# Performance work log

Hardware: AMD Instinct MI355X
Metric: run time of the kernel (lower is better)

Reference implementation:

```python
import jax, jax.numpy as jnp
import numpy as np

L, S, N, E, H = 1024, 1024, 4, 1024, 16


def setup_inputs() -> dict:
    key = jax.random.key(0)
    ks = jax.random.split(key, 7)
    return {
        "query": jax.random.normal(ks[0], (L, N, E), jnp.float32),
        "key": jax.random.normal(ks[1], (S, N, E), jnp.float32),
        "value": jax.random.normal(ks[2], (S, N, E), jnp.float32),
        "in_proj_weight": jax.random.normal(ks[3], (3 * E, E), jnp.float32) * (E ** -0.5),
        "in_proj_bias": jax.random.normal(ks[4], (3 * E,), jnp.float32) * 0.02,
        "out_proj_weight": jax.random.normal(ks[5], (E, E), jnp.float32) * (E ** -0.5),
        "out_proj_bias": jax.random.normal(ks[6], (E,), jnp.float32) * 0.02,
        "num_heads": H,
    }


def _split_heads(x, n, h, hd):
    # (T, N, E) -> (N*h, T, hd), matching torch view(T, N*h, hd).transpose(0, 1)
    t = x.shape[0]
    return jnp.transpose(x.reshape(t, n * h, hd), (1, 0, 2))


def reference(query, key, value, in_proj_weight, in_proj_bias,
              out_proj_weight, out_proj_bias, num_heads):
    tgt_len, bsz, embed_dim = query.shape
    src_len = key.shape[0]
    head_dim = embed_dim // num_heads
    scaling = float(head_dim) ** -0.5

    # packed QKV projection (torch F.linear: x @ W.T + b), sliced as in source
    q = query @ in_proj_weight[:embed_dim].T + in_proj_bias[:embed_dim]
    k = key @ in_proj_weight[embed_dim:2 * embed_dim].T + in_proj_bias[embed_dim:2 * embed_dim]
    v = value @ in_proj_weight[2 * embed_dim:].T + in_proj_bias[2 * embed_dim:]
    q = q * scaling

    q = _split_heads(q, bsz, num_heads, head_dim)  # (N*H, L, hd)
    k = _split_heads(k, bsz, num_heads, head_dim)  # (N*H, S, hd)
    v = _split_heads(v, bsz, num_heads, head_dim)  # (N*H, S, hd)

    scores = jnp.einsum('bld,bsd->bls', q, k)           # (N*H, L, S)
    attn = jax.nn.softmax(scores, axis=-1)
    ctx = jnp.einsum('bls,bsd->bld', attn, v)           # (N*H, L, hd)

    # (N*H, L, hd) -> (L, N, E)
    ctx = jnp.transpose(ctx, (1, 0, 2)).reshape(tgt_len, bsz, embed_dim)
    attn_output = ctx @ out_proj_weight.T + out_proj_bias

    # need_weights=True path: average over heads -> (N, L, S)
    attn_weights = attn.reshape(bsz, num_heads, tgt_len, src_len).sum(axis=1) / num_heads
    return attn_output, attn_weights
```

## Files before the change

kernel.cpp:

```cpp
#include <hip/hip_runtime.h>

typedef unsigned short u16;
typedef __attribute__((ext_vector_type(8))) short short8;
typedef __attribute__((ext_vector_type(4))) float f32x4;

__device__ __forceinline__ u16 f2bf(float f) {
  unsigned int i = __float_as_uint(f);
  i += 0x7fffu + ((i >> 16) & 1u);
  return (u16)(i >> 16);
}

__device__ __forceinline__ short8 cvt8(const float* p) {
  float4 a = ((const float4*)p)[0];
  float4 b = ((const float4*)p)[1];
  short8 r;
  r[0] = (short)f2bf(a.x); r[1] = (short)f2bf(a.y);
  r[2] = (short)f2bf(a.z); r[3] = (short)f2bf(a.w);
  r[4] = (short)f2bf(b.x); r[5] = (short)f2bf(b.y);
  r[6] = (short)f2bf(b.z); r[7] = (short)f2bf(b.w);
  return r;
}

__global__ __launch_bounds__(256) void convert_bf16(
    const float* __restrict__ q, const float* __restrict__ k,
    const float* __restrict__ v, const float* __restrict__ Wi,
    const float* __restrict__ Wo,
    u16* __restrict__ qb, u16* __restrict__ kb, u16* __restrict__ vb,
    u16* __restrict__ Wib, u16* __restrict__ Wob)
{
  const float* src; u16* dst; int len8;
  switch (blockIdx.y) {
    case 0:  src = q;  dst = qb;  len8 = 524288; break;
    case 1:  src = k;  dst = kb;  len8 = 524288; break;
    case 2:  src = v;  dst = vb;  len8 = 524288; break;
    case 3:  src = Wi; dst = Wib; len8 = 393216; break;
    default: src = Wo; dst = Wob; len8 = 131072; break;
  }
  int stride = gridDim.x * 256;
  for (int i = blockIdx.x * 256 + threadIdx.x; i < len8; i += stride)
    *(short8*)(dst + (size_t)i * 8) = cvt8(src + (size_t)i * 8);
}

__global__ __launch_bounds__(256) void qkv_gemm(
    const u16* __restrict__ qb, const u16* __restrict__ kb,
    const u16* __restrict__ vb, const u16* __restrict__ W,
    const float* __restrict__ bias,
    u16* __restrict__ qh, u16* __restrict__ kh, u16* __restrict__ vt)
{
  __shared__ __align__(16) u16 As[128 * 64];
  __shared__ __align__(16) u16 Bs[128 * 64];

  const int tid  = threadIdx.x;
  const int wave = tid >> 6;
  const int lane = tid & 63;
  const int r    = lane & 15;
  const int q4   = lane >> 4;
  const int wm   = wave >> 1;
  const int wn   = wave & 1;

  const int orig = blockIdx.y * 24 + blockIdx.x;
  const int nid  = (orig & 7) * 96 + (orig >> 3);
  const int mt   = nid / 24;
  const int jt   = nid - mt * 24;
  const int src  = jt >> 3;
  const u16* X = (src == 0) ? qb : (src == 1) ? kb : vb;
  const int m0 = mt * 128;
  const int j0 = jt * 128;

  const int ls   = lane >> 3;
  const int swzb = ((lane & 7) ^ ls) << 4;
  const char* Xc = (const char*)X;
  const char* Wc = (const char*)W;

  f32x4 acc[4][4];
  #pragma unroll
  for (int a = 0; a < 4; ++a)
    #pragma unroll
    for (int b = 0; b < 4; ++b)
      acc[a][b] = (f32x4){0.f, 0.f, 0.f, 0.f};

  for (int kt = 0; kt < 16; ++kt) {
    const int kb2 = kt * 128;
    __syncthreads();
    #pragma unroll
    for (int i = 0; i < 4; ++i) {
      const int row = wave * 32 + i * 8 + ls;
      __builtin_amdgcn_global_load_lds(
          (const u16*)(Xc + (size_t)(m0 + row) * 2048 + kb2 + swzb),
          As + (wave * 4 + i) * 512, 16, 0, 0);
      __builtin_amdgcn_global_load_lds(
          (const u16*)(Wc + (size_t)(j0 + row) * 2048 + kb2 + swzb),
          Bs + (wave * 4 + i) * 512, 16, 0, 0);
    }
    __syncthreads();

    #pragma unroll
    for (int ks = 0; ks < 2; ++ks) {
      short8 af[4], bf[4];
      #pragma unroll
      for (int mi = 0; mi < 4; ++mi) {
        const int row = wm * 64 + mi * 16 + r;
        af[mi] = *(const short8*)(As + row * 64 + ((((ks << 2) | q4) ^ (r & 7)) << 3));
      }
      #pragma unroll
      for (int ji = 0; ji < 4; ++ji) {
        const int row = wn * 64 + ji * 16 + r;
        bf[ji] = *(const short8*)(Bs + row * 64 + ((((ks << 2) | q4) ^ (r & 7)) << 3));
      }
      #pragma unroll
      for (int mi = 0; mi < 4; ++mi)
        #pragma unroll
        for (int ji = 0; ji < 4; ++ji)
          acc[mi][ji] = __builtin_amdgcn_mfma_f32_16x16x32_bf16(af[mi], bf[ji], acc[mi][ji], 0, 0, 0);
    }
  }

  #pragma unroll
  for (int mi = 0; mi < 4; ++mi) {
    #pragma unroll
    for (int ji = 0; ji < 4; ++ji) {
      #pragma unroll
      for (int rr = 0; rr < 4; ++rr) {
        int m = m0 + wm * 64 + mi * 16 + q4 * 4 + rr;
        int j = j0 + wn * 64 + ji * 16 + r;
        float v = acc[mi][ji][rr] + bias[j];
        int t = m >> 2, n = m & 3;
        int jj = j & 1023;
        int h = jj >> 6, d = jj & 63;
        int bb = n * 16 + h;
        if (src == 0)
          qh[(size_t)bb * 65536 + (size_t)t * 64 + d] = f2bf(v * 0.125f);
        else if (src == 1)
          kh[(size_t)bb * 65536 + (size_t)t * 64 + d] = f2bf(v);
        else
          vt[(size_t)bb * 65536 + (size_t)d * 1024 + t] = f2bf(v);
      }
    }
  }
}

__global__ __launch_bounds__(256) void attn_ctx_mfma(
    const u16* __restrict__ qh, const u16* __restrict__ kh,
    const u16* __restrict__ vt, u16* __restrict__ ctx,
    float* __restrict__ Zbuf)
{
  __shared__ __align__(16) u16 Ks[2][4096];
  __shared__ __align__(16) u16 Vs[2][4096];
  __shared__ __align__(16) u16 Pl[4][1024];

  const int tid = threadIdx.x;
  const int wv = tid >> 6, lane = tid & 63, r = lane & 15, q4 = lane >> 4;
  const int b  = blockIdx.y;
  const int lw = blockIdx.x * 64 + wv * 16;
  const int n = b >> 4, h = b & 15;

  const u16* qbase = qh + (size_t)b * 65536;
  const char* kc = (const char*)(kh + (size_t)b * 65536);
  const char* vc = (const char*)(vt + (size_t)b * 65536);
  u16* P = Pl[wv];

  const int ls  = lane >> 3;
  const int swzb = ((lane & 7) ^ ls) << 4;
  const int iw  = wv * 2;
  const size_t klo = (size_t)iw * 1024 + (size_t)ls * 128 + swzb;
  const size_t vlo = (size_t)iw * 16384 + (size_t)ls * 2048 + swzb;

  const int rsw = r & 7;
  const int c0 = (q4 ^ rsw) << 3;
  const int c1 = ((q4 ^ rsw) ^ 4) << 3;

  short8 aq0 = *(const short8*)(qbase + (size_t)(lw + r) * 64 + q4 * 8);
  short8 aq1 = *(const short8*)(qbase + (size_t)(lw + r) * 64 + 32 + q4 * 8);

  f32x4 oc[4];
  #pragma unroll
  for (int ji = 0; ji < 4; ++ji) oc[ji] = (f32x4){0.f, 0.f, 0.f, 0.f};
  float z[4] = {0.f, 0.f, 0.f, 0.f};

  {
    const char* kp = kc + klo;
    const char* vp = vc + vlo;
    u16* kd = &Ks[0][iw * 512];
    u16* vd = &Vs[0][iw * 512];
    __builtin_amdgcn_global_load_lds(kp,          kd,       16, 0, 0);
    __builtin_amdgcn_global_load_lds(kp + 1024,   kd + 512, 16, 0, 0);
    __builtin_amdgcn_global_load_lds(vp,          vd,       16, 0, 0);
    __builtin_amdgcn_global_load_lds(vp + 16384,  vd + 512, 16, 0, 0);
  }

  for (int it = 0; it < 16; ++it) {
    const int cur = it & 1;
    __syncthreads();
    const u16* Kb = Ks[cur];
    const u16* Vb = Vs[cur];

    f32x4 sc[4];
    #pragma unroll
    for (int ji = 0; ji < 4; ++ji) {
      const int row = (ji * 16 + r) * 64;
      short8 bk0 = *(const short8*)(Kb + row + c0);
      short8 bk1 = *(const short8*)(Kb + row + c1);
      f32x4 t = (f32x4){0.f, 0.f, 0.f, 0.f};
      t = __builtin_amdgcn_mfma_f32_16x16x32_bf16(aq0, bk0, t, 0, 0, 0);
      t = __builtin_amdgcn_mfma_f32_16x16x32_bf16(aq1, bk1, t, 0, 0, 0);
      sc[ji] = t;
    }

    if (it < 15) {
      const char* kp = kc + (size_t)(it + 1) * 8192 + klo;
      const char* vp = vc + (size_t)(it + 1) * 128  + vlo;
      u16* kd = &Ks[cur ^ 1][iw * 512];
      u16* vd = &Vs[cur ^ 1][iw * 512];
      __builtin_amdgcn_global_load_lds(kp,          kd,       16, 0, 0);
      __builtin_amdgcn_global_load_lds(kp + 1024,   kd + 512, 16, 0, 0);
      __builtin_amdgcn_global_load_lds(vp,          vd,       16, 0, 0);
      __builtin_amdgcn_global_load_lds(vp + 16384,  vd + 512, 16, 0, 0);
    }

    #pragma unroll
    for (int ji = 0; ji < 4; ++ji) {
      const int cw = ji * 2 + (r >> 3);
      #pragma unroll
      for (int rr = 0; rr < 4; ++rr) {
        float e = __expf(sc[ji][rr]);
        z[rr] += e;
        const int row = q4 * 4 + rr;
        P[row * 64 + ((cw ^ (row & 7)) << 3) + (r & 7)] = f2bf(e);
      }
    }
    asm volatile("s_waitcnt lgkmcnt(0)" ::: "memory");
    short8 ap0 = *(const short8*)(P + r * 64 + c0);
    short8 ap1 = *(const short8*)(P + r * 64 + c1);
    #pragma unroll
    for (int ji = 0; ji < 4; ++ji) {
      const int row = (ji * 16 + r) * 64;
      short8 bv0 = *(const short8*)(Vb + row + c0);
      short8 bv1 = *(const short8*)(Vb + row + c1);
      oc[ji] = __builtin_amdgcn_mfma_f32_16x16x32_bf16(ap0, bv0, oc[ji], 0, 0, 0);
      oc[ji] = __builtin_amdgcn_mfma_f32_16x16x32_bf16(ap1, bv1, oc[ji], 0, 0, 0);
    }
  }

  #pragma unroll
  for (int rr = 0; rr < 4; ++rr) {
    float zz = z[rr];
    zz += __shfl_xor(zz, 1);
    zz += __shfl_xor(zz, 2);
    zz += __shfl_xor(zz, 4);
    zz += __shfl_xor(zz, 8);
    z[rr] = zz;
  }

  #pragma unroll
  for (int rr = 0; rr < 4; ++rr) {
    float inv = 1.0f / z[rr];
    int l = lw + q4 * 4 + rr;
    u16* crow = ctx + ((size_t)l * 4 + n) * 1024 + h * 64;
    #pragma unroll
    for (int ji = 0; ji < 4; ++ji)
      crow[ji * 16 + r] = f2bf(oc[ji][rr] * inv);
    if (r == 0) Zbuf[(size_t)b * 1024 + l] = z[rr];
  }
}

__global__ __launch_bounds__(256) void attn_w_mfma(
    const u16* __restrict__ qh, const u16* __restrict__ kh,
    const float* __restrict__ Zbuf, float* __restrict__ out_w)
{
  __shared__ __align__(16) u16 Kw[2][4096];
  __shared__ float invZ[16][64];

  const int tid = threadIdx.x;
  const int wv = tid >> 6, lane = tid & 63, r = lane & 15, q4 = lane >> 4;
  const int lt = blockIdx.x;
  const int st = blockIdx.y;
  const int n  = blockIdx.z;
  const int l0 = lt * 64;
  const int s0 = st * 64;
  const int lw = l0 + wv * 16;

  const char* khc = (const char*)kh + (size_t)n * 2097152;

  const int ls  = lane >> 3;
  const int swzb = ((lane & 7) ^ ls) << 4;
  const int iw  = wv * 2;
  const size_t klo = (size_t)s0 * 128 + (size_t)iw * 1024 + (size_t)ls * 128 + swzb;

  const int rsw = r & 7;
  const int c0 = (q4 ^ rsw) << 3;
  const int c1 = ((q4 ^ rsw) ^ 4) << 3;

  for (int i = tid; i < 1024; i += 256) {
    int hh = i >> 6, row = i & 63;
    invZ[hh][row] = 1.0f / (Zbuf[(size_t)(n * 16 + hh) * 1024 + l0 + row] * 16.0f);
  }

  {
    const char* kp = khc + klo;
    u16* kd = &Kw[0][iw * 512];
    __builtin_amdgcn_global_load_lds(kp,        kd,       16, 0, 0);
    __builtin_amdgcn_global_load_lds(kp + 1024, kd + 512, 16, 0, 0);
  }
  const u16* q0 = qh + (size_t)(n * 16) * 65536;
  short8 aqc0 = *(const short8*)(q0 + (size_t)(lw + r) * 64 + q4 * 8);
  short8 aqc1 = *(const short8*)(q0 + (size_t)(lw + r) * 64 + 32 + q4 * 8);

  f32x4 wacc[4];
  #pragma unroll
  for (int ji = 0; ji < 4; ++ji) wacc[ji] = (f32x4){0.f, 0.f, 0.f, 0.f};

  for (int hh = 0; hh < 16; ++hh) {
    const int cur = hh & 1;
    __syncthreads();
    if (hh < 15) {
      const char* kp = khc + (size_t)(hh + 1) * 131072 + klo;
      u16* kd = &Kw[cur ^ 1][iw * 512];
      __builtin_amdgcn_global_load_lds(kp,        kd,       16, 0, 0);
      __builtin_amdgcn_global_load_lds(kp + 1024, kd + 512, 16, 0, 0);
    }
    const int hn = (hh < 15) ? hh + 1 : hh;
    const u16* qn = qh + (size_t)(n * 16 + hn) * 65536;
    short8 an0 = *(const short8*)(qn + (size_t)(lw + r) * 64 + q4 * 8);
    short8 an1 = *(const short8*)(qn + (size_t)(lw + r) * 64 + 32 + q4 * 8);

    const u16* Kb = Kw[cur];
    f32x4 sc[4];
    #pragma unroll
    for (int ji = 0; ji < 4; ++ji) {
      const int row = (ji * 16 + r) * 64;
      short8 bk0 = *(const short8*)(Kb + row + c0);
      short8 bk1 = *(const short8*)(Kb + row + c1);
      f32x4 t = (f32x4){0.f, 0.f, 0.f, 0.f};
      t = __builtin_amdgcn_mfma_f32_16x16x32_bf16(aqc0, bk0, t, 0, 0, 0);
      t = __builtin_amdgcn_mfma_f32_16x16x32_bf16(aqc1, bk1, t, 0, 0, 0);
      sc[ji] = t;
    }
    #pragma unroll
    for (int rr = 0; rr < 4; ++rr) {
      float iv = invZ[hh][wv * 16 + q4 * 4 + rr];
      #pragma unroll
      for (int ji = 0; ji < 4; ++ji)
        wacc[ji][rr] += __expf(sc[ji][rr]) * iv;
    }
    aqc0 = an0; aqc1 = an1;
  }

  #pragma unroll
  for (int ji = 0; ji < 4; ++ji)
    #pragma unroll
    for (int rr = 0; rr < 4; ++rr) {
      int row = lw + q4 * 4 + rr;
      int col = s0 + ji * 16 + r;
      out_w[(size_t)n * 1048576 + (size_t)row * 1024 + col] = wacc[ji][rr];
    }
}

__global__ __launch_bounds__(256) void out_gemm(
    const u16* __restrict__ ctx, const u16* __restrict__ W,
    const float* __restrict__ bias, float* __restrict__ out)
{
  __shared__ __align__(16) u16 As[128 * 64];
  __shared__ __align__(16) u16 Bs[64 * 64];

  const int tid  = threadIdx.x;
  const int wave = tid >> 6;
  const int lane = tid & 63;
  const int r    = lane & 15;
  const int q4   = lane >> 4;
  const int wm   = wave >> 1;
  const int wn   = wave & 1;

  const int orig = blockIdx.y * 16 + blockIdx.x;
  const int nid  = (orig & 7) * 64 + (orig >> 3);
  const int mt   = nid >> 4;
  const int jt   = nid & 15;
  const int m0 = mt * 128;
  const int j0 = jt * 64;

  const int ls   = lane >> 3;
  const int swzb = ((lane & 7) ^ ls) << 4;
  const char* Ac = (const char*)ctx;
  const char* Wc = (const char*)W;

  f32x4 acc[4][2];
  #pragma unroll
  for (int a = 0; a < 4; ++a)
    #pragma unroll
    for (int b = 0; b < 2; ++b)
      acc[a][b] = (f32x4){0.f, 0.f, 0.f, 0.f};

  for (int kt = 0; kt < 16; ++kt) {
    const int kb2 = kt * 128;
    __syncthreads();
    #pragma unroll
    for (int i = 0; i < 4; ++i) {
      const int row = wave * 32 + i * 8 + ls;
      __builtin_amdgcn_global_load_lds(
          (const u16*)(Ac + (size_t)(m0 + row) * 2048 + kb2 + swzb),
          As + (wave * 4 + i) * 512, 16, 0, 0);
    }
    #pragma unroll
    for (int i = 0; i < 2; ++i) {
      const int row = wave * 16 + i * 8 + ls;
      __builtin_amdgcn_global_load_lds(
          (const u16*)(Wc + (size_t)(j0 + row) * 2048 + kb2 + swzb),
          Bs + (wave * 2 + i) * 512, 16, 0, 0);
    }
    __syncthreads();

    #pragma unroll
    for (int ks = 0; ks < 2; ++ks) {
      short8 af[4], bf[2];
      #pragma unroll
      for (int mi = 0; mi < 4; ++mi) {
        const int row = wm * 64 + mi * 16 + r;
        af[mi] = *(const short8*)(As + row * 64 + ((((ks << 2) | q4) ^ (r & 7)) << 3));
      }
      #pragma unroll
      for (int ji = 0; ji < 2; ++ji) {
        const int row = wn * 32 + ji * 16 + r;
        bf[ji] = *(const short8*)(Bs + row * 64 + ((((ks << 2) | q4) ^ (r & 7)) << 3));
      }
      #pragma unroll
      for (int mi = 0; mi < 4; ++mi)
        #pragma unroll
        for (int ji = 0; ji < 2; ++ji)
          acc[mi][ji] = __builtin_amdgcn_mfma_f32_16x16x32_bf16(af[mi], bf[ji], acc[mi][ji], 0, 0, 0);
    }
  }

  #pragma unroll
  for (int mi = 0; mi < 4; ++mi) {
    #pragma unroll
    for (int ji = 0; ji < 2; ++ji) {
      #pragma unroll
      for (int rr = 0; rr < 4; ++rr) {
        int m = m0 + wm * 64 + mi * 16 + q4 * 4 + rr;
        int j = j0 + wn * 32 + ji * 16 + r;
        out[(size_t)m * 1024 + j] = acc[mi][ji][rr] + bias[j];
      }
    }
  }
}

extern "C" void kernel_launch(void* const* d_in, const int* in_sizes, int n_in,
                              void* d_out, int out_size, void* d_ws, size_t ws_size,
                              hipStream_t stream) {
  const float* query = (const float*)d_in[0];
  const float* key   = (const float*)d_in[1];
  const float* value = (const float*)d_in[2];
  const float* W_in  = (const float*)d_in[3];
  const float* b_in  = (const float*)d_in[4];
  const float* W_out = (const float*)d_in[5];
  const float* b_out = (const float*)d_in[6];
  float* out = (float*)d_out;

  u16* qb  = (u16*)d_ws;
  u16* kb  = qb  + (size_t)4194304;
  u16* vb  = kb  + (size_t)4194304;
  u16* Wib = vb  + (size_t)4194304;
  u16* Wob = Wib + (size_t)3145728;
  u16* qh  = Wob + (size_t)1048576;
  u16* kh  = qh  + (size_t)4194304;
  u16* vt  = kh  + (size_t)4194304;
  u16* ctx = vt  + (size_t)4194304;
  float* Zbuf = (float*)(ctx + (size_t)4194304);

  convert_bf16<<<dim3(512, 5), 256, 0, stream>>>(query, key, value, W_in, W_out,
                                                 qb, kb, vb, Wib, Wob);
  qkv_gemm<<<dim3(24, 32), 256, 0, stream>>>(qb, kb, vb, Wib, b_in, qh, kh, vt);
  attn_ctx_mfma<<<dim3(16, 64), 256, 0, stream>>>(qh, kh, vt, ctx, Zbuf);
  attn_w_mfma<<<dim3(16, 16, 4), 256, 0, stream>>>(qh, kh, Zbuf, out + (size_t)4194304);
  out_gemm<<<dim3(16, 32), 256, 0, stream>>>(ctx, Wob, b_out, out);
}
```

Measured before the change: 246.1 us.

## Double-buffer LDS tiles with K=32 stages in QKV and output GEMMs

Both projection GEMMs now use two LDS buffers with half-width K tiles (32 instead of 64). Each iteration starts the async global-to-LDS load for the next K slice before running the MFMAs on the current one, with a new XOR swizzle for the narrower rows. This overlaps global memory latency with matrix compute and cuts the barriers to one per iteration. The cost is twice as many loop iterations, each with less MFMA work per barrier, while total LDS use stays the same.

```diff
diff --git a/kernel.cpp b/kernel.cpp
--- a/kernel.cpp
+++ b/kernel.cpp
@@ -47,8 +47,8 @@
     const float* __restrict__ bias,
     u16* __restrict__ qh, u16* __restrict__ kh, u16* __restrict__ vt)
 {
-  __shared__ __align__(16) u16 As[128 * 64];
-  __shared__ __align__(16) u16 Bs[128 * 64];
+  __shared__ __align__(16) u16 As[2][128 * 32];
+  __shared__ __align__(16) u16 Bs[2][128 * 32];
 
   const int tid  = threadIdx.x;
   const int wave = tid >> 6;
@@ -67,11 +67,13 @@
   const int m0 = mt * 128;
   const int j0 = jt * 128;
 
-  const int ls   = lane >> 3;
-  const int swzb = ((lane & 7) ^ ls) << 4;
+  const int lrow = lane >> 2;
+  const int lchk = ((lane & 3) ^ ((lane >> 3) & 3)) << 4;
   const char* Xc = (const char*)X;
   const char* Wc = (const char*)W;
 
+  const int fchk = (q4 ^ ((r >> 1) & 3)) << 3;
+
   f32x4 acc[4][4];
   #pragma unroll
   for (int a = 0; a < 4; ++a)
@@ -79,40 +81,38 @@
     for (int b = 0; b < 4; ++b)
       acc[a][b] = (f32x4){0.f, 0.f, 0.f, 0.f};
 
-  for (int kt = 0; kt < 16; ++kt) {
-    const int kb2 = kt * 128;
+  auto STAGE = [&](int buf, int kt) {
+    const int kbyte = kt * 64;
+    #pragma unroll
+    for (int i = 0; i < 2; ++i) {
+      const int g = wave * 2 + i;
+      __builtin_amdgcn_global_load_lds(
+          (const u16*)(Xc + (size_t)(m0 + g * 16 + lrow) * 2048 + kbyte + lchk),
+          &As[buf][g * 512], 16, 0, 0);
+      __builtin_amdgcn_global_load_lds(
+          (const u16*)(Wc + (size_t)(j0 + g * 16 + lrow) * 2048 + kbyte + lchk),
+          &Bs[buf][g * 512], 16, 0, 0);
+    }
+  };
+
+  STAGE(0, 0);
+  for (int kt = 0; kt < 32; ++kt) {
+    const int cur = kt & 1;
     __syncthreads();
-    #pragma unroll
-    for (int i = 0; i < 4; ++i) {
-      const int row = wave * 32 + i * 8 + ls;
-      __builtin_amdgcn_global_load_lds(
-          (const u16*)(Xc + (size_t)(m0 + row) * 2048 + kb2 + swzb),
-          As + (wave * 4 + i) * 512, 16, 0, 0);
-      __builtin_amdgcn_global_load_lds(
-          (const u16*)(Wc + (size_t)(j0 + row) * 2048 + kb2 + swzb),
-          Bs + (wave * 4 + i) * 512, 16, 0, 0);
-    }
-    __syncthreads();
-
-    #pragma unroll
-    for (int ks = 0; ks < 2; ++ks) {
-      short8 af[4], bf[4];
-      #pragma unroll
-      for (int mi = 0; mi < 4; ++mi) {
-        const int row = wm * 64 + mi * 16 + r;
-        af[mi] = *(const short8*)(As + row * 64 + ((((ks << 2) | q4) ^ (r & 7)) << 3));
-      }
-      #pragma unroll
-      for (int ji = 0; ji < 4; ++ji) {
-        const int row = wn * 64 + ji * 16 + r;
-        bf[ji] = *(const short8*)(Bs + row * 64 + ((((ks << 2) | q4) ^ (r & 7)) << 3));
-      }
-      #pragma unroll
-      for (int mi = 0; mi < 4; ++mi)
-        #pragma unroll
-        for (int ji = 0; ji < 4; ++ji)
-          acc[mi][ji] = __builtin_amdgcn_mfma_f32_16x16x32_bf16(af[mi], bf[ji], acc[mi][ji], 0, 0, 0);
-    }
+    if (kt < 31) STAGE(cur ^ 1, kt + 1);
+
+    short8 af[4], bf[4];
+    #pragma unroll
+    for (int mi = 0; mi < 4; ++mi)
+      af[mi] = *(const short8*)(&As[cur][(wm * 64 + mi * 16 + r) * 32 + fchk]);
+    #pragma unroll
+    for (int ji = 0; ji < 4; ++ji)
+      bf[ji] = *(const short8*)(&Bs[cur][(wn * 64 + ji * 16 + r) * 32 + fchk]);
+    #pragma unroll
+    for (int mi = 0; mi < 4; ++mi)
+      #pragma unroll
+      for (int ji = 0; ji < 4; ++ji)
+        acc[mi][ji] = __builtin_amdgcn_mfma_f32_16x16x32_bf16(af[mi], bf[ji], acc[mi][ji], 0, 0, 0);
   }
 
   #pragma unroll
@@ -359,8 +359,8 @@
     const u16* __restrict__ ctx, const u16* __restrict__ W,
     const float* __restrict__ bias, float* __restrict__ out)
 {
-  __shared__ __align__(16) u16 As[128 * 64];
-  __shared__ __align__(16) u16 Bs[64 * 64];
+  __shared__ __align__(16) u16 As[2][128 * 32];
+  __shared__ __align__(16) u16 Bs[2][64 * 32];
 
   const int tid  = threadIdx.x;
   const int wave = tid >> 6;
@@ -377,10 +377,11 @@
   const int m0 = mt * 128;
   const int j0 = jt * 64;
 
-  const int ls   = lane >> 3;
-  const int swzb = ((lane & 7) ^ ls) << 4;
+  const int lrow = lane >> 2;
+  const int lchk = ((lane & 3) ^ ((lane >> 3) & 3)) << 4;
   const char* Ac = (const char*)ctx;
   const char* Wc = (const char*)W;
+  const int fchk = (q4 ^ ((r >> 1) & 3)) << 3;
 
   f32x4 acc[4][2];
   #pragma unroll
@@ -389,44 +390,38 @@
     for (int b = 0; b < 2; ++b)
       acc[a][b] = (f32x4){0.f, 0.f, 0.f, 0.f};
 
-  for (int kt = 0; kt < 16; ++kt) {
-    const int kb2 = kt * 128;
+  auto STAGE = [&](int buf, int kt) {
+    const int kbyte = kt * 64;
+    #pragma unroll
+    for (int i = 0; i < 2; ++i) {
+      const int g = wave * 2 + i;
+      __builtin_amdgcn_global_load_lds(
+          (const u16*)(Ac + (size_t)(m0 + g * 16 + lrow) * 2048 + kbyte + lchk),
+          &As[buf][g * 512], 16, 0, 0);
+    }
+    __builtin_amdgcn_global_load_lds(
+        (const u16*)(Wc + (size_t)(j0 + wave * 16 + lrow) * 2048 + kbyte + lchk),
+        &Bs[buf][wave * 512], 16, 0, 0);
+  };
+
+  STAGE(0, 0);
+  for (int kt = 0; kt < 32; ++kt) {
+    const int cur = kt & 1;
     __syncthreads();
-    #pragma unroll
-    for (int i = 0; i < 4; ++i) {
-      const int row = wave * 32 + i * 8 + ls;
-      __builtin_amdgcn_global_load_lds(
-          (const u16*)(Ac + (size_t)(m0 + row) * 2048 + kb2 + swzb),
-          As + (wave * 4 + i) * 512, 16, 0, 0);
-    }
-    #pragma unroll
-    for (int i = 0; i < 2; ++i) {
-      const int row = wave * 16 + i * 8 + ls;
-      __builtin_amdgcn_global_load_lds(
-          (const u16*)(Wc + (size_t)(j0 + row) * 2048 + kb2 + swzb),
-          Bs + (wave * 2 + i) * 512, 16, 0, 0);
-    }
-    __syncthreads();
-
-    #pragma unroll
-    for (int ks = 0; ks < 2; ++ks) {
-      short8 af[4], bf[2];
-      #pragma unroll
-      for (int mi = 0; mi < 4; ++mi) {
-        const int row = wm * 64 + mi * 16 + r;
-        af[mi] = *(const short8*)(As + row * 64 + ((((ks << 2) | q4) ^ (r & 7)) << 3));
-      }
-      #pragma unroll
-      for (int ji = 0; ji < 2; ++ji) {
-        const int row = wn * 32 + ji * 16 + r;
-        bf[ji] = *(const short8*)(Bs + row * 64 + ((((ks << 2) | q4) ^ (r & 7)) << 3));
-      }
-      #pragma unroll
-      for (int mi = 0; mi < 4; ++mi)
-        #pragma unroll
-        for (int ji = 0; ji < 2; ++ji)
-          acc[mi][ji] = __builtin_amdgcn_mfma_f32_16x16x32_bf16(af[mi], bf[ji], acc[mi][ji], 0, 0, 0);
-    }
+    if (kt < 31) STAGE(cur ^ 1, kt + 1);
+
+    short8 af[4], bf[2];
+    #pragma unroll
+    for (int mi = 0; mi < 4; ++mi)
+      af[mi] = *(const short8*)(&As[cur][(wm * 64 + mi * 16 + r) * 32 + fchk]);
+    #pragma unroll
+    for (int ji = 0; ji < 2; ++ji)
+      bf[ji] = *(const short8*)(&Bs[cur][(wn * 32 + ji * 16 + r) * 32 + fchk]);
+    #pragma unroll
+    for (int mi = 0; mi < 4; ++mi)
+      #pragma unroll
+      for (int ji = 0; ji < 2; ++ji)
+        acc[mi][ji] = __builtin_amdgcn_mfma_f32_16x16x32_bf16(af[mi], bf[ji], acc[mi][ji], 0, 0, 0);
   }
 
   #pragma unroll
```

New measurement: 245.6 us. About the same (-0.2%).
